# Kernel tuning notes

Hardware: AMD Instinct MI355X
Metric: run time of the kernel (lower is better)

The kernel has to match this reference:

```python
import jax, jax.numpy as jnp
import numpy as np

N_NODES = 100000
IN_CH = 65
HID_CH = 64
N_EDGES = 3200000


def setup_inputs() -> dict:
    key = jax.random.key(0)
    k1, k2, k3, k4, k5 = jax.random.split(key, 5)
    x = jax.random.normal(k1, (N_NODES, IN_CH), dtype=jnp.float32)
    edge_index = jax.random.randint(k2, (2, N_EDGES), 0, N_NODES, dtype=jnp.int64)
    edge_weight = jax.random.uniform(k3, (N_EDGES,), dtype=jnp.float32)
    # PyG GraphConv params: lin_rel (with bias) applied to aggregated neighbors,
    # lin_root (no bias) applied to self features.
    scale = 1.0 / np.sqrt(IN_CH)
    W_rel = jax.random.uniform(k4, (HID_CH, IN_CH), dtype=jnp.float32, minval=-scale, maxval=scale)
    b_rel = jnp.zeros((HID_CH,), dtype=jnp.float32)
    W_root = jax.random.uniform(k5, (HID_CH, IN_CH), dtype=jnp.float32, minval=-scale, maxval=scale)
    return {"x": x, "edge_index": edge_index, "edge_weight": edge_weight,
            "W_rel": W_rel, "b_rel": b_rel, "W_root": W_root}


def reference(x, edge_index, edge_weight, W_rel, b_rel, W_root):
    src = edge_index[0]  # source nodes (x_j in PyG message)
    dst = edge_index[1]  # target nodes (aggregation index)
    # gather neighbor features, weight by edge weight: [E, IN_CH]
    msgs = x[src] * edge_weight[:, None]
    # scatter-add to destination nodes: [N, IN_CH]
    aggr = jax.ops.segment_sum(msgs, dst, num_segments=N_NODES)
    # out = lin_rel(aggr) + lin_root(x)
    out = aggr @ W_rel.T + b_rel + x @ W_root.T
    return out
```

## Files before the change

### kernel.cpp

```cpp
#include <hip/hip_runtime.h>

#define IN_CH 65
#define HID 64
#define BN 64
#define NB 1563
#define CAP 2560
#define SCAP 2432
#define EPB 8192
#define TPS 1024
#define EPT (EPB / TPS)

static inline size_t align16(size_t v) { return (v + 15) & ~(size_t)15; }

__device__ inline ushort f2bf(float f) {
    uint u = __float_as_uint(f);
    return (ushort)((u + 0x7FFF + ((u >> 16) & 1)) >> 16);
}
__device__ inline float bf2f(ushort h) { return __uint_as_float((uint)h << 16); }

__global__ __launch_bounds__(256) void k1(const float* __restrict__ x,
                                          const float* __restrict__ W_rel,
                                          const float* __restrict__ b_rel,
                                          const float* __restrict__ W_root,
                                          ushort* __restrict__ y16,
                                          float* __restrict__ out,
                                          int* __restrict__ cnt, int nBuckets,
                                          int nNodes) {
    __shared__ float xs[64 * IN_CH];
    __shared__ float ws[IN_CH * 128];
    const int tid = threadIdx.x;
    const int tx = tid & 15;
    const int ty = tid >> 4;
    const long nodeBase = (long)blockIdx.x * 64;
    const int nValid = min(64, nNodes - (int)nodeBase);
    const int nx = nValid * IN_CH;

    if (cnt && tid == 0 && blockIdx.x < (unsigned)nBuckets) cnt[blockIdx.x] = 0;

    for (int i = tid; i < IN_CH * 128; i += 256) {
        const int c = i >> 7, j = i & 127;
        ws[i] = (j < HID) ? W_rel[j * IN_CH + c] : W_root[(j - HID) * IN_CH + c];
    }
    const float* xsrc = x + nodeBase * IN_CH;
    for (int i = tid; i < 64 * IN_CH; i += 256) xs[i] = (i < nx) ? xsrc[i] : 0.f;
    __syncthreads();

    float acc[4][8];
#pragma unroll
    for (int i = 0; i < 4; ++i)
#pragma unroll
        for (int j = 0; j < 8; ++j) acc[i][j] = 0.f;

    const int r0 = ty * 4;
    const int c0 = tx * 8;
    for (int k = 0; k < IN_CH; ++k) {
        float aa[4] = {xs[(r0 + 0) * IN_CH + k], xs[(r0 + 1) * IN_CH + k],
                       xs[(r0 + 2) * IN_CH + k], xs[(r0 + 3) * IN_CH + k]};
        float4 b0 = *(const float4*)&ws[k * 128 + c0];
        float4 b1 = *(const float4*)&ws[k * 128 + c0 + 4];
        float bb[8] = {b0.x, b0.y, b0.z, b0.w, b1.x, b1.y, b1.z, b1.w};
#pragma unroll
        for (int i = 0; i < 4; ++i)
#pragma unroll
            for (int j = 0; j < 8; ++j) acc[i][j] += aa[i] * bb[j];
    }

    if (c0 >= HID) {
        const int h0 = c0 - HID;
        float4 bb0 = *(const float4*)&b_rel[h0];
        float4 bb1 = *(const float4*)&b_rel[h0 + 4];
        float bv[8] = {bb0.x, bb0.y, bb0.z, bb0.w, bb1.x, bb1.y, bb1.z, bb1.w};
#pragma unroll
        for (int i = 0; i < 4; ++i)
#pragma unroll
            for (int j = 0; j < 8; ++j) acc[i][j] += bv[j];
    }

#pragma unroll
    for (int i = 0; i < 4; ++i) {
        const long node = nodeBase + r0 + i;
        if (node >= nNodes) break;
        if (c0 < HID) {
            uint4 pk;
            pk.x = (uint)f2bf(acc[i][0]) | ((uint)f2bf(acc[i][1]) << 16);
            pk.y = (uint)f2bf(acc[i][2]) | ((uint)f2bf(acc[i][3]) << 16);
            pk.z = (uint)f2bf(acc[i][4]) | ((uint)f2bf(acc[i][5]) << 16);
            pk.w = (uint)f2bf(acc[i][6]) | ((uint)f2bf(acc[i][7]) << 16);
            *(uint4*)&y16[node * HID + c0] = pk;
        } else {
            float* dst = out + node * HID + (c0 - HID);
            *(float4*)(dst + 0) = make_float4(acc[i][0], acc[i][1], acc[i][2], acc[i][3]);
            *(float4*)(dst + 4) = make_float4(acc[i][4], acc[i][5], acc[i][6], acc[i][7]);
        }
    }
}

__global__ __launch_bounds__(TPS) void scatterB(const int* __restrict__ ei,
                                                const float* __restrict__ ew,
                                                int* __restrict__ cnt,
                                                int2* __restrict__ pairs, int E) {
    __shared__ int lhist[NB];
    __shared__ int lbase[NB];
    const int tid = threadIdx.x;
    const long e0 = (long)blockIdx.x * EPB;
    const int n = (int)min((long)EPB, (long)E - e0);

    for (int i = tid; i < NB; i += TPS) lhist[i] = 0;
    __syncthreads();

    int dstv[EPT], srcv[EPT];
    float wv[EPT];
#pragma unroll
    for (int k = 0; k < EPT; ++k) {
        const int i = tid + k * TPS;
        const bool valid = i < n;
        dstv[k] = valid ? ei[(long)E + e0 + i] : 0;
        srcv[k] = valid ? ei[e0 + i] : 0;
        wv[k]   = valid ? ew[e0 + i] : 0.f;
        if (valid) atomicAdd(&lhist[dstv[k] >> 6], 1);
    }
    __syncthreads();

    for (int i = tid; i < NB; i += TPS) {
        const int c = lhist[i];
        lbase[i] = c ? atomicAdd(&cnt[i], c) : 0;
        lhist[i] = 0;
    }
    __syncthreads();

#pragma unroll
    for (int k = 0; k < EPT; ++k) {
        const int i = tid + k * TPS;
        if (i < n) {
            const int b = dstv[k] >> 6;
            const int p = lbase[b] + atomicAdd(&lhist[b], 1);
            if (p < CAP)
                pairs[(size_t)b * CAP + p] =
                    make_int2(srcv[k] | ((dstv[k] & (BN - 1)) << 17),
                              __float_as_int(wv[k]));
        }
    }
}

__global__ __launch_bounds__(512) void aggregateS16(const int2* __restrict__ pairs,
                                                    const int* __restrict__ cnt,
                                                    const ushort* __restrict__ y16,
                                                    float* __restrict__ out, int N) {
    __shared__ int2 sorted[SCAP];
    __shared__ int sH[BN];
    __shared__ int soff[BN + 1];
    __shared__ int scur[BN];
    const int tid = threadIdx.x;
    const int lane = tid & 63;
    const int wv = tid >> 6;
    const int b = blockIdx.x;

    if (tid < BN) { sH[tid] = 0; scur[tid] = 0; }
    __syncthreads();

    const int m = min(cnt[b], CAP);
    const int2* pb = pairs + (size_t)b * CAP;

    for (int i = tid; i < m; i += 512)
        atomicAdd(&sH[pb[i].x >> 17], 1);
    __syncthreads();

    for (int off = 1; off < BN; off <<= 1) {
        int v = 0;
        if (tid < BN) {
            v = sH[tid];
            if (tid >= off) v += sH[tid - off];
        }
        __syncthreads();
        if (tid < BN) sH[tid] = v;
        __syncthreads();
    }
    if (tid < BN) soff[tid + 1] = sH[tid];
    if (tid == 0) soff[0] = 0;
    __syncthreads();

    for (int i = tid; i < m; i += 512) {
        const int2 p = pb[i];
        const int d = p.x >> 17;
        const int slot = soff[d] + atomicAdd(&scur[d], 1);
        if (slot < SCAP) sorted[slot] = make_int2(p.x & 0x1FFFF, p.y);
    }
    __syncthreads();

    const long nodeBase = (long)b * BN;
    for (int nl = wv; nl < BN; nl += 8) {
        const long node = nodeBase + nl;
        if (node >= N) break;
        const int kbeg = min(soff[nl], SCAP);
        const int kend = min(soff[nl + 1], SCAP);
        float acc = 0.f;
        int k = kbeg;
        for (; k + 4 <= kend; k += 4) {
            const int2 p0 = sorted[k], p1 = sorted[k + 1];
            const int2 p2 = sorted[k + 2], p3 = sorted[k + 3];
            const float v0 = bf2f(y16[(size_t)p0.x * HID + lane]);
            const float v1 = bf2f(y16[(size_t)p1.x * HID + lane]);
            const float v2 = bf2f(y16[(size_t)p2.x * HID + lane]);
            const float v3 = bf2f(y16[(size_t)p3.x * HID + lane]);
            acc += __int_as_float(p0.y) * v0;
            acc += __int_as_float(p1.y) * v1;
            acc += __int_as_float(p2.y) * v2;
            acc += __int_as_float(p3.y) * v3;
        }
        for (; k < kend; ++k) {
            const int2 p = sorted[k];
            acc += __int_as_float(p.y) * bf2f(y16[(size_t)p.x * HID + lane]);
        }
        out[node * HID + lane] += acc;
    }
}

__global__ __launch_bounds__(256) void k2_atomic16(const int* __restrict__ ei,
                                                   const float* __restrict__ ew,
                                                   const ushort* __restrict__ y16,
                                                   float* __restrict__ out, int E) {
    const long t = (long)blockIdx.x * 256 + threadIdx.x;
    const long e = t >> 4;
    const int r = (int)(t & 15);
    if (e >= E) return;
    const int src = ei[e];
    const int dst = ei[(long)E + e];
    const float w = ew[e];
    const uint2 q = ((const uint2*)y16)[(size_t)src * 16 + r];
    float* o = out + (size_t)dst * HID + r * 4;
    unsafeAtomicAdd(o + 0, w * __uint_as_float(q.x << 16));
    unsafeAtomicAdd(o + 1, w * __uint_as_float(q.x & 0xFFFF0000u));
    unsafeAtomicAdd(o + 2, w * __uint_as_float(q.y << 16));
    unsafeAtomicAdd(o + 3, w * __uint_as_float(q.y & 0xFFFF0000u));
}

extern "C" void kernel_launch(void* const* d_in, const int* in_sizes, int n_in,
                              void* d_out, int out_size, void* d_ws, size_t ws_size,
                              hipStream_t stream) {
    const float* x      = (const float*)d_in[0];
    const int*   ei     = (const int*)d_in[1];
    const float* ew     = (const float*)d_in[2];
    const float* W_rel  = (const float*)d_in[3];
    const float* b_rel  = (const float*)d_in[4];
    const float* W_root = (const float*)d_in[5];
    float* out = (float*)d_out;

    const int N = in_sizes[0] / IN_CH;
    const int E = in_sizes[2];

    char* base = (char*)d_ws;
    const size_t oY     = 0;
    const size_t oPairs = align16((size_t)N * HID * 2);
    const size_t oCnt   = oPairs + align16((size_t)NB * CAP * 8);
    const size_t need   = oCnt + (size_t)NB * 4;

    ushort* y16 = (ushort*)(base + oY);
    const int nb1 = (N + 63) / 64;

    const bool fits = (ws_size >= need) && (N <= (1 << 17)) &&
                      ((size_t)NB * BN >= (size_t)N) && ((long)E <= (long)N * 33) &&
                      (nb1 >= NB);

    if (fits) {
        int2* pairs = (int2*)(base + oPairs);
        int*  cnt   = (int*)(base + oCnt);

        k1<<<nb1, 256, 0, stream>>>(x, W_rel, b_rel, W_root, y16, out, cnt, NB, N);
        scatterB<<<(E + EPB - 1) / EPB, TPS, 0, stream>>>(ei, ew, cnt, pairs, E);
        aggregateS16<<<NB, 512, 0, stream>>>(pairs, cnt, y16, out, N);
    } else {
        k1<<<nb1, 256, 0, stream>>>(x, W_rel, b_rel, W_root, y16, out,
                                    (int*)nullptr, 0, N);
        const long thr2 = (long)E * 16;
        k2_atomic16<<<(int)((thr2 + 255) / 256), 256, 0, stream>>>(ei, ew, y16, out, E);
    }
}
```

Measured before the change: 267.1 us.

## Split wavefront across two edges with packed bf16x2 loads in aggregation

The aggregation kernel now has each half of a 64-lane wavefront process alternate edges. Each lane loads a packed pair of bf16 values with one 32-bit load instead of one 16-bit element, and the two halves are combined with a cross-lane shuffle before a float2 store. The source index is pre-shifted into a byte offset when packing pairs, which removes per-load index multiplies. The weight tile in shared memory is padded to a stride of 132 and loaded with coalesced reads from the weight matrices, to reduce bank conflicts and uncoalesced global reads. The packing trick relies on node ids fitting in 17 bits and the destination-local id in the top bits.

```diff
diff --git a/kernel.cpp b/kernel.cpp
--- a/kernel.cpp
+++ b/kernel.cpp
@@ -9,6 +9,7 @@
 #define EPB 8192
 #define TPS 1024
 #define EPT (EPB / TPS)
+#define WSTR 132
 
 static inline size_t align16(size_t v) { return (v + 15) & ~(size_t)15; }
 
@@ -27,7 +28,7 @@
                                           int* __restrict__ cnt, int nBuckets,
                                           int nNodes) {
     __shared__ float xs[64 * IN_CH];
-    __shared__ float ws[IN_CH * 128];
+    __shared__ float ws[IN_CH * WSTR];
     const int tid = threadIdx.x;
     const int tx = tid & 15;
     const int ty = tid >> 4;
@@ -37,9 +38,13 @@
 
     if (cnt && tid == 0 && blockIdx.x < (unsigned)nBuckets) cnt[blockIdx.x] = 0;
 
-    for (int i = tid; i < IN_CH * 128; i += 256) {
-        const int c = i >> 7, j = i & 127;
-        ws[i] = (j < HID) ? W_rel[j * IN_CH + c] : W_root[(j - HID) * IN_CH + c];
+    for (int f = tid; f < HID * IN_CH; f += 256) {
+        const int j = f / IN_CH, c = f - j * IN_CH;
+        ws[c * WSTR + j] = W_rel[f];
+    }
+    for (int f = tid; f < HID * IN_CH; f += 256) {
+        const int j = f / IN_CH, c = f - j * IN_CH;
+        ws[c * WSTR + HID + j] = W_root[f];
     }
     const float* xsrc = x + nodeBase * IN_CH;
     for (int i = tid; i < 64 * IN_CH; i += 256) xs[i] = (i < nx) ? xsrc[i] : 0.f;
@@ -56,8 +61,8 @@
     for (int k = 0; k < IN_CH; ++k) {
         float aa[4] = {xs[(r0 + 0) * IN_CH + k], xs[(r0 + 1) * IN_CH + k],
                        xs[(r0 + 2) * IN_CH + k], xs[(r0 + 3) * IN_CH + k]};
-        float4 b0 = *(const float4*)&ws[k * 128 + c0];
-        float4 b1 = *(const float4*)&ws[k * 128 + c0 + 4];
+        float4 b0 = *(const float4*)&ws[k * WSTR + c0];
+        float4 b1 = *(const float4*)&ws[k * WSTR + c0 + 4];
         float bb[8] = {b0.x, b0.y, b0.z, b0.w, b1.x, b1.y, b1.z, b1.w};
 #pragma unroll
         for (int i = 0; i < 4; ++i)
@@ -136,7 +141,7 @@
             const int p = lbase[b] + atomicAdd(&lhist[b], 1);
             if (p < CAP)
                 pairs[(size_t)b * CAP + p] =
-                    make_int2(srcv[k] | ((dstv[k] & (BN - 1)) << 17),
+                    make_int2((srcv[k] << 7) | ((dstv[k] & (BN - 1)) << 25),
                               __float_as_int(wv[k]));
         }
     }
@@ -153,6 +158,8 @@
     const int tid = threadIdx.x;
     const int lane = tid & 63;
     const int wv = tid >> 6;
+    const int half = lane >> 5;
+    const uint lane4 = (lane & 31) * 4;
     const int b = blockIdx.x;
 
     if (tid < BN) { sH[tid] = 0; scur[tid] = 0; }
@@ -162,7 +169,7 @@
     const int2* pb = pairs + (size_t)b * CAP;
 
     for (int i = tid; i < m; i += 512)
-        atomicAdd(&sH[pb[i].x >> 17], 1);
+        atomicAdd(&sH[(uint)pb[i].x >> 25], 1);
     __syncthreads();
 
     for (int off = 1; off < BN; off <<= 1) {
@@ -181,37 +188,53 @@
 
     for (int i = tid; i < m; i += 512) {
         const int2 p = pb[i];
-        const int d = p.x >> 17;
+        const int d = (uint)p.x >> 25;
         const int slot = soff[d] + atomicAdd(&scur[d], 1);
-        if (slot < SCAP) sorted[slot] = make_int2(p.x & 0x1FFFF, p.y);
-    }
-    __syncthreads();
-
+        if (slot < SCAP) sorted[slot] = make_int2(p.x & 0x00FFFF80, p.y);
+    }
+    __syncthreads();
+
+    const char* yb = (const char*)y16;
     const long nodeBase = (long)b * BN;
     for (int nl = wv; nl < BN; nl += 8) {
         const long node = nodeBase + nl;
         if (node >= N) break;
         const int kbeg = min(soff[nl], SCAP);
         const int kend = min(soff[nl + 1], SCAP);
-        float acc = 0.f;
-        int k = kbeg;
-        for (; k + 4 <= kend; k += 4) {
-            const int2 p0 = sorted[k], p1 = sorted[k + 1];
-            const int2 p2 = sorted[k + 2], p3 = sorted[k + 3];
-            const float v0 = bf2f(y16[(size_t)p0.x * HID + lane]);
-            const float v1 = bf2f(y16[(size_t)p1.x * HID + lane]);
-            const float v2 = bf2f(y16[(size_t)p2.x * HID + lane]);
-            const float v3 = bf2f(y16[(size_t)p3.x * HID + lane]);
-            acc += __int_as_float(p0.y) * v0;
-            acc += __int_as_float(p1.y) * v1;
-            acc += __int_as_float(p2.y) * v2;
-            acc += __int_as_float(p3.y) * v3;
-        }
-        for (; k < kend; ++k) {
+        float ax = 0.f, ay = 0.f;
+        int k = kbeg + half;
+        for (; k + 6 < kend; k += 8) {
+            const int2 p0 = sorted[k],     p1 = sorted[k + 2];
+            const int2 p2 = sorted[k + 4], p3 = sorted[k + 6];
+            const uint q0 = *(const uint*)(yb + (uint)p0.x + lane4);
+            const uint q1 = *(const uint*)(yb + (uint)p1.x + lane4);
+            const uint q2 = *(const uint*)(yb + (uint)p2.x + lane4);
+            const uint q3 = *(const uint*)(yb + (uint)p3.x + lane4);
+            const float w0 = __int_as_float(p0.y), w1 = __int_as_float(p1.y);
+            const float w2 = __int_as_float(p2.y), w3 = __int_as_float(p3.y);
+            ax += w0 * __uint_as_float(q0 << 16);
+            ay += w0 * __uint_as_float(q0 & 0xFFFF0000u);
+            ax += w1 * __uint_as_float(q1 << 16);
+            ay += w1 * __uint_as_float(q1 & 0xFFFF0000u);
+            ax += w2 * __uint_as_float(q2 << 16);
+            ay += w2 * __uint_as_float(q2 & 0xFFFF0000u);
+            ax += w3 * __uint_as_float(q3 << 16);
+            ay += w3 * __uint_as_float(q3 & 0xFFFF0000u);
+        }
+        for (; k < kend; k += 2) {
             const int2 p = sorted[k];
-            acc += __int_as_float(p.y) * bf2f(y16[(size_t)p.x * HID + lane]);
-        }
-        out[node * HID + lane] += acc;
+            const uint q = *(const uint*)(yb + (uint)p.x + lane4);
+            const float w = __int_as_float(p.y);
+            ax += w * __uint_as_float(q << 16);
+            ay += w * __uint_as_float(q & 0xFFFF0000u);
+        }
+        ax += __shfl_xor(ax, 32);
+        ay += __shfl_xor(ay, 32);
+        if (half == 0) {
+            float2* o = (float2*)(out + node * HID) + (lane & 31);
+            const float2 cur = *o;
+            *o = make_float2(cur.x + ax, cur.y + ay);
+        }
     }
 }
 
```

New measurement: 249.7 us. 1.07x faster.
